# Kernel tuning notes

Hardware: AMD Instinct MI355X
Metric: run time of the kernel (lower is better)

Reference implementation:

```python
import jax, jax.numpy as jnp
import numpy as np

STATE_DIM = 256
LATENT_DIM = 64
HIDDEN = 64
NUM_EMB = 2048
BATCH = 32768


def setup_inputs() -> dict:
    key = jax.random.key(0)
    ks = jax.random.split(key, 10)
    s = lambda *sh: 1.0 / np.sqrt(sh[0])
    return {
        "x": jax.random.normal(ks[0], (BATCH, STATE_DIM), dtype=jnp.float32),
        # encoder: Linear(state_dim, 64) -> ReLU -> Linear(64, latent_dim)
        "enc_w1": jax.random.uniform(ks[1], (STATE_DIM, HIDDEN), jnp.float32, -s(STATE_DIM), s(STATE_DIM)),
        "enc_b1": jax.random.uniform(ks[2], (HIDDEN,), jnp.float32, -s(STATE_DIM), s(STATE_DIM)),
        "enc_w2": jax.random.uniform(ks[3], (HIDDEN, LATENT_DIM), jnp.float32, -s(HIDDEN), s(HIDDEN)),
        "enc_b2": jax.random.uniform(ks[4], (LATENT_DIM,), jnp.float32, -s(HIDDEN), s(HIDDEN)),
        # codebook
        "emb": jax.random.normal(ks[5], (NUM_EMB, LATENT_DIM), dtype=jnp.float32),
        # decoder: Linear(latent_dim, 64) -> ReLU -> Linear(64, state_dim)
        "dec_w1": jax.random.uniform(ks[6], (LATENT_DIM, HIDDEN), jnp.float32, -s(LATENT_DIM), s(LATENT_DIM)),
        "dec_b1": jax.random.uniform(ks[7], (HIDDEN,), jnp.float32, -s(LATENT_DIM), s(LATENT_DIM)),
        "dec_w2": jax.random.uniform(ks[8], (HIDDEN, STATE_DIM), jnp.float32, -s(HIDDEN), s(HIDDEN)),
        "dec_b2": jax.random.uniform(ks[9], (STATE_DIM,), jnp.float32, -s(HIDDEN), s(HIDDEN)),
    }


def reference(x, enc_w1, enc_b1, enc_w2, enc_b2, emb, dec_w1, dec_b1, dec_w2, dec_b2):
    # encoder MLP: z_e [B, latent]
    h = jax.nn.relu(x @ enc_w1 + enc_b1)
    z_e = h @ enc_w2 + enc_b2
    # squared euclidean distances to codebook, expanded form: [B, K]
    # ||z - e||^2 = ||z||^2 - 2 z.e + ||e||^2  (same argmin as broadcast form)
    d = (jnp.sum(z_e * z_e, axis=1, keepdims=True)
         - 2.0 * (z_e @ emb.T)
         + jnp.sum(emb * emb, axis=1)[None, :])
    z_q_idx = jnp.argmin(d, axis=1)           # [B]
    z_q = emb[z_q_idx]                        # [B, latent]
    # decoder MLP
    hd = jax.nn.relu(z_q @ dec_w1 + dec_b1)
    x_recon = hd @ dec_w2 + dec_b2
    return (x_recon, z_e, z_q)
```

## Files before the change

kernel.cpp:

```cpp
#include <hip/hip_runtime.h>

#define BATCH   32768
#define SD      256
#define LD      64
#define HDIM    64
#define NEMB    2048
#define REFINE_THR_Q 5e-4f

typedef short  short8 __attribute__((ext_vector_type(8)));
typedef float  f32x4  __attribute__((ext_vector_type(4)));

__device__ __forceinline__ unsigned short f2bf(float f) {
    unsigned int u = __float_as_uint(f);
    u = (u + 0x7FFFu + ((u >> 16) & 1u)) >> 16;
    return (unsigned short)u;
}
__device__ __forceinline__ float bf2f(unsigned short h) {
    return __uint_as_float(((unsigned int)h) << 16);
}

__global__ __launch_bounds__(256) void k0_all(const float* __restrict__ emb,
                                              const float* __restrict__ dw1,
                                              const float* __restrict__ dw2,
                                              float* __restrict__ e2q,
                                              unsigned short* __restrict__ eh,
                                              unsigned short* __restrict__ el,
                                              unsigned short* __restrict__ w1h,
                                              unsigned short* __restrict__ w1l,
                                              unsigned short* __restrict__ w2h,
                                              unsigned short* __restrict__ w2l,
                                              int* __restrict__ count) {
    int b = blockIdx.x;
    int t = threadIdx.x;
    if (b < 8) {
        int k = b * 256 + t;
        if (k == 0) *count = 0;
        const float* er = emb + (size_t)k * LD;
        unsigned short hrow[LD], lrow[LD];
        float s = 0.f;
#pragma unroll
        for (int q = 0; q < LD; ++q) {
            float v = er[q];
            s += v * v;
            unsigned short h = f2bf(v);
            hrow[q] = h;
            lrow[q] = f2bf(v - bf2f(h));
        }
        e2q[k] = -0.5f * s;
        short8* dh = (short8*)(eh + (size_t)k * LD);
        short8* dl = (short8*)(el + (size_t)k * LD);
#pragma unroll
        for (int q = 0; q < 8; ++q) {
            dh[q] = *(short8*)&hrow[q * 8];
            dl[q] = *(short8*)&lrow[q * 8];
        }
    } else if (b < 24) {
        int e = (b - 8) * 256 + t;
        int j = e >> 6, k = e & 63;
        float v = dw1[k * HDIM + j];
        unsigned short h = f2bf(v);
        w1h[e] = h; w1l[e] = f2bf(v - bf2f(h));
    } else {
        int e = (b - 24) * 256 + t;
        int j = e >> 6, k = e & 63;
        float v = dw2[k * SD + j];
        unsigned short h = f2bf(v);
        w2h[e] = h; w2l[e] = f2bf(v - bf2f(h));
    }
}

__global__ __launch_bounds__(512, 4) void k_enc(const float* __restrict__ x,
                                                const float* __restrict__ w1,
                                                const float* __restrict__ b1,
                                                const float* __restrict__ w2,
                                                const float* __restrict__ b2,
                                                float* __restrict__ zOut,
                                                unsigned short* __restrict__ zh,
                                                unsigned short* __restrict__ zl) {
    __shared__ float smem[20480];
    float* w1s = smem;
    float* xs  = smem + 16384;
    int tid = threadIdx.x;
    {
        const float4* src = (const float4*)w1;
        float4* dst = (float4*)w1s;
#pragma unroll
        for (int t = 0; t < 8; ++t) dst[tid + 512 * t] = src[tid + 512 * t];
    }
    int r0 = blockIdx.x * 64;
    int sr = tid >> 3;
    int sq = tid & 7;
    const float* xrow = x + (size_t)(r0 + sr) * SD + sq * 4;
    *(float4*)&xs[sr * 32 + sq * 4] = *(const float4*)xrow;
    __syncthreads();

    int lane = tid & 63;
    int w = tid >> 6;
    float acc[8];
#pragma unroll
    for (int r = 0; r < 8; ++r) acc[r] = 0.f;

    for (int c = 0; c < 8; ++c) {
        float4 nv;
        if (c < 7) nv = *(const float4*)(xrow + (c + 1) * 32);
        const float* xb = &xs[(c & 1) * 2048 + (w * 8) * 32];
        int kb = c * 32;
#pragma unroll
        for (int i0 = 0; i0 < 32; i0 += 8) {
            float wf[8];
#pragma unroll
            for (int jj = 0; jj < 8; ++jj) wf[jj] = w1s[(kb + i0 + jj) * HDIM + lane];
#pragma unroll
            for (int r = 0; r < 8; ++r) {
                const float* xr = xb + r * 32 + i0;
                float4 xa = *(const float4*)xr;
                float4 xc = *(const float4*)(xr + 4);
                acc[r] += xa.x * wf[0] + xa.y * wf[1] + xa.z * wf[2] + xa.w * wf[3]
                        + xc.x * wf[4] + xc.y * wf[5] + xc.z * wf[6] + xc.w * wf[7];
            }
        }
        __syncthreads();
        if (c < 7) *(float4*)&xs[((c + 1) & 1) * 2048 + sr * 32 + sq * 4] = nv;
        __syncthreads();
    }

    float* hs  = smem;
    float* w2s = smem + 4096;
    float bb1 = b1[lane];
#pragma unroll
    for (int r = 0; r < 8; ++r)
        hs[(w * 8 + r) * 64 + lane] = fmaxf(acc[r] + bb1, 0.f);
    {
        const float4* src = (const float4*)w2;
        float4* dst = (float4*)w2s;
        dst[tid] = src[tid];
        dst[tid + 512] = src[tid + 512];
    }
    __syncthreads();

    const float* hb = &hs[(w * 8) * 64];
    float ac2[8];
#pragma unroll
    for (int r = 0; r < 8; ++r) ac2[r] = 0.f;

    for (int j0 = 0; j0 < HDIM; j0 += 8) {
        float wf[8];
#pragma unroll
        for (int jj = 0; jj < 8; ++jj) wf[jj] = w2s[(j0 + jj) * LD + lane];
#pragma unroll
        for (int r = 0; r < 8; ++r) {
            const float* hr = hb + r * 64 + j0;
            float4 ha = *(const float4*)hr;
            float4 hc = *(const float4*)(hr + 4);
            ac2[r] += ha.x * wf[0] + ha.y * wf[1] + ha.z * wf[2] + ha.w * wf[3]
                    + hc.x * wf[4] + hc.y * wf[5] + hc.z * wf[6] + hc.w * wf[7];
        }
    }
    float bb2 = b2[lane];
#pragma unroll
    for (int r = 0; r < 8; ++r) {
        float z = ac2[r] + bb2;
        size_t o = (size_t)(r0 + w * 8 + r) * LD + lane;
        zOut[o] = z;
        unsigned short h = f2bf(z);
        zh[o] = h;
        zl[o] = f2bf(z - bf2f(h));
    }
}

#define K2_LOAD(P, t) do {                                                  \
    const unsigned short* ph_ = ehp + (size_t)(t) * 16 * LD;                \
    const unsigned short* pl_ = elp + (size_t)(t) * 16 * LD;                \
    P##a0 = *(const short8*)(ph_);                                          \
    P##a1 = *(const short8*)(ph_ + 32);                                     \
    P##a2 = *(const short8*)(pl_);                                          \
    P##a3 = *(const short8*)(pl_ + 32);                                     \
    P##e2 = *(const f32x4*)(e2q + cbase + (t) * 16 + hi * 4);               \
} while (0)

#define K2_COMP(P, t) do {                                                  \
    f32x4 acc_[4];                                                          \
    _Pragma("unroll")                                                       \
    for (int g = 0; g < 4; ++g) {                                           \
        f32x4 c_;                                                           \
        c_ = __builtin_amdgcn_mfma_f32_16x16x32_bf16(P##a0, bh[g][0], P##e2, 0, 0, 0); \
        c_ = __builtin_amdgcn_mfma_f32_16x16x32_bf16(P##a1, bh[g][1], c_, 0, 0, 0);    \
        c_ = __builtin_amdgcn_mfma_f32_16x16x32_bf16(P##a2, bh[g][0], c_, 0, 0, 0);    \
        c_ = __builtin_amdgcn_mfma_f32_16x16x32_bf16(P##a3, bh[g][1], c_, 0, 0, 0);    \
        c_ = __builtin_amdgcn_mfma_f32_16x16x32_bf16(P##a0, bl[g][0], c_, 0, 0, 0);    \
        c_ = __builtin_amdgcn_mfma_f32_16x16x32_bf16(P##a1, bl[g][1], c_, 0, 0, 0);    \
        acc_[g] = c_;                                                       \
    }                                                                       \
    _Pragma("unroll")                                                       \
    for (int g = 0; g < 4; ++g) {                                           \
        float m_ = fmaxf(fmaxf(acc_[g][0], acc_[g][1]),                     \
                         fmaxf(acc_[g][2], acc_[g][3]));                    \
        bool win_ = (m_ > bb[g]);                                           \
        qv[g] = win_ ? acc_[g] : qv[g];                                     \
        tt[g] = win_ ? (t) : tt[g];                                         \
        b2v[g] = fmaxf(b2v[g], fminf(bb[g], m_));                           \
        bb[g] = fmaxf(bb[g], m_);                                           \
    }                                                                       \
} while (0)

__global__ __launch_bounds__(256, 2) void k2_mfma(const unsigned short* __restrict__ zh,
                                                  const unsigned short* __restrict__ zl,
                                                  const unsigned short* __restrict__ eh,
                                                  const unsigned short* __restrict__ el,
                                                  const float* __restrict__ e2q,
                                                  int* __restrict__ idx,
                                                  int* __restrict__ list,
                                                  int* __restrict__ count) {
    int tid  = threadIdx.x;
    int lane = tid & 63;
    int w    = tid >> 6;
    int rb   = blockIdx.x * 64;
    int lo   = lane & 15;
    int hi   = lane >> 4;

    short8 bh[4][2], bl[4][2];
#pragma unroll
    for (int g = 0; g < 4; ++g) {
        size_t zo = (size_t)(rb + g * 16 + lo) * LD + hi * 8;
        bh[g][0] = *(const short8*)(zh + zo);
        bh[g][1] = *(const short8*)(zh + zo + 32);
        bl[g][0] = *(const short8*)(zl + zo);
        bl[g][1] = *(const short8*)(zl + zo + 32);
    }

    float bb[4], b2v[4];
    f32x4 qv[4];
    int   tt[4];
#pragma unroll
    for (int g = 0; g < 4; ++g) {
        bb[g] = -3.0e38f; b2v[g] = -3.0e38f; tt[g] = 0;
        qv[g][0] = qv[g][1] = qv[g][2] = qv[g][3] = -3.0e38f;
    }

    const int cbase = w * (NEMB / 4);
    const unsigned short* ehp = eh + (size_t)(cbase + lo) * LD + hi * 8;
    const unsigned short* elp = el + (size_t)(cbase + lo) * LD + hi * 8;

    short8 Aa0, Aa1, Aa2, Aa3; f32x4 Ae2;
    short8 Ba0, Ba1, Ba2, Ba3; f32x4 Be2;
    short8 Ca0, Ca1, Ca2, Ca3; f32x4 Ce2;

    K2_LOAD(A, 0);
    K2_LOAD(B, 1);
    K2_LOAD(C, 2);

    for (int tb = 0; tb < 27; tb += 3) {
        K2_COMP(A, tb);     K2_LOAD(A, tb + 3);
        K2_COMP(B, tb + 1); K2_LOAD(B, tb + 4);
        K2_COMP(C, tb + 2); K2_LOAD(C, tb + 5);
    }
    K2_COMP(A, 27); K2_LOAD(A, 30);
    K2_COMP(B, 28); K2_LOAD(B, 31);
    K2_COMP(C, 29);
    K2_COMP(A, 30);
    K2_COMP(B, 31);

    float ss[4];
    int   ii[4];
#pragma unroll
    for (int g = 0; g < 4; ++g) {
        float s0 = qv[g][0], s1 = qv[g][1], s2 = qv[g][2], s3 = qv[g][3];
        float M01 = fmaxf(s0, s1), L01 = fminf(s0, s1);
        float M23 = fmaxf(s2, s3), L23 = fminf(s2, s3);
        int   d01 = (s1 > s0) ? 1 : 0;
        int   d23 = (s3 > s2) ? 3 : 2;
        bool  cp  = (M23 > M01);
        float within2 = fmaxf(fminf(M01, M23), cp ? L23 : L01);
        int   dd  = cp ? d23 : d01;
        ii[g] = cbase + tt[g] * 16 + hi * 4 + dd;
        ss[g] = fmaxf(b2v[g], within2);
    }

#pragma unroll
    for (int off = 16; off <= 32; off <<= 1) {
#pragma unroll
        for (int g = 0; g < 4; ++g) {
            float ob = __shfl_xor(bb[g], off);
            float os = __shfl_xor(ss[g], off);
            int   oi = __shfl_xor(ii[g], off);
            ss[g] = fmaxf(fmaxf(fminf(bb[g], ob), os), ss[g]);
            ii[g] = (ob > bb[g]) ? oi : ii[g];
            bb[g] = fmaxf(bb[g], ob);
        }
    }

    __shared__ float Lb[4][64];
    __shared__ float Ls[4][64];
    __shared__ int   Li[4][64];
    if (lane < 16) {
#pragma unroll
        for (int g = 0; g < 4; ++g) {
            Lb[w][g * 16 + lane] = bb[g];
            Ls[w][g * 16 + lane] = ss[g];
            Li[w][g * 16 + lane] = ii[g];
        }
    }
    __syncthreads();

    if (tid < 64) {
        float B = Lb[0][tid], S = Ls[0][tid];
        int   I = Li[0][tid];
#pragma unroll
        for (int w2 = 1; w2 < 4; ++w2) {
            float ob = Lb[w2][tid], os = Ls[w2][tid];
            int   oi = Li[w2][tid];
            S = fmaxf(fmaxf(fminf(B, ob), os), S);
            I = (ob > B) ? oi : I;
            B = fmaxf(B, ob);
        }
        idx[rb + tid] = I;
        if (B - S < REFINE_THR_Q) {
            int p = atomicAdd(count, 1);
            list[p] = rb + tid;
        }
    }
}

__global__ __launch_bounds__(256) void k3_refine(const float* __restrict__ z,
                                                 const float* __restrict__ emb,
                                                 const int* __restrict__ count,
                                                 const int* __restrict__ list,
                                                 int* __restrict__ idx) {
    __shared__ double sv[256];
    __shared__ int    sx[256];
    int tid = threadIdx.x;
    int n = *count;
    for (int g = blockIdx.x; g < n; g += gridDim.x) {
        int row = list[g];
        const float4* zr4 = (const float4*)(z + (size_t)row * LD);
        float4 zv[16];
#pragma unroll
        for (int q = 0; q < 16; ++q) zv[q] = zr4[q];

        double best = 1.0e300;
        int bi = NEMB;
#pragma unroll 2
        for (int c = 0; c < 8; ++c) {
            int k = tid * 8 + c;
            const float4* er = (const float4*)(emb + (size_t)k * LD);
            double d0 = 0.0, d1 = 0.0, d2 = 0.0, d3 = 0.0;
#pragma unroll
            for (int q = 0; q < 16; ++q) {
                float4 e4 = er[q];
                double tx = (double)zv[q].x - (double)e4.x;
                double ty = (double)zv[q].y - (double)e4.y;
                double tz = (double)zv[q].z - (double)e4.z;
                double tw = (double)zv[q].w - (double)e4.w;
                d0 += tx * tx; d1 += ty * ty; d2 += tz * tz; d3 += tw * tw;
            }
            double d = (d0 + d1) + (d2 + d3);
            if (d < best) { best = d; bi = k; }
        }
        sv[tid] = best; sx[tid] = bi;
        __syncthreads();
        for (int s = 128; s > 0; s >>= 1) {
            if (tid < s) {
                if (sv[tid + s] < sv[tid] ||
                    (sv[tid + s] == sv[tid] && sx[tid + s] < sx[tid])) {
                    sv[tid] = sv[tid + s]; sx[tid] = sx[tid + s];
                }
            }
            __syncthreads();
        }
        if (tid == 0) idx[row] = sx[0];
        __syncthreads();
    }
}

__global__ __launch_bounds__(256, 2) void k_dec(const int* __restrict__ idx,
                                                const float* __restrict__ emb,
                                                const unsigned short* __restrict__ w1h,
                                                const unsigned short* __restrict__ w1l,
                                                const float* __restrict__ b1,
                                                const unsigned short* __restrict__ w2h,
                                                const unsigned short* __restrict__ w2l,
                                                const float* __restrict__ b2,
                                                float* __restrict__ xrec,
                                                float* __restrict__ zq) {
    __shared__ float hds[4][16 * 68];
    int tid  = threadIdx.x;
    int lane = tid & 63;
    int w    = tid >> 6;
    int lo   = lane & 15;
    int hi   = lane >> 4;
    int rb   = blockIdx.x * 64 + w * 16;
    int row  = rb + lo;
    int ix   = idx[row];

    short8 zah[2], zal[2];
    {
        const float* er  = emb + (size_t)ix * LD + hi * 8;
        float* zqr = zq + (size_t)row * LD + hi * 8;
#pragma unroll
        for (int kt = 0; kt < 2; ++kt) {
            float4 a = *(const float4*)(er + kt * 32);
            float4 b = *(const float4*)(er + kt * 32 + 4);
            *(float4*)(zqr + kt * 32) = a;
            *(float4*)(zqr + kt * 32 + 4) = b;
            float v[8] = {a.x, a.y, a.z, a.w, b.x, b.y, b.z, b.w};
            unsigned short hh[8], ll[8];
#pragma unroll
            for (int q = 0; q < 8; ++q) {
                unsigned short hb = f2bf(v[q]);
                hh[q] = hb;
                ll[q] = f2bf(v[q] - bf2f(hb));
            }
            zah[kt] = *(short8*)hh;
            zal[kt] = *(short8*)ll;
        }
    }

#pragma unroll
    for (int jt = 0; jt < 4; ++jt) {
        float bj = b1[jt * 16 + lo];
        f32x4 c = {bj, bj, bj, bj};
#pragma unroll
        for (int kt = 0; kt < 2; ++kt) {
            short8 bh8 = *(const short8*)(w1h + (jt * 16 + lo) * LD + kt * 32 + hi * 8);
            short8 bl8 = *(const short8*)(w1l + (jt * 16 + lo) * LD + kt * 32 + hi * 8);
            c = __builtin_amdgcn_mfma_f32_16x16x32_bf16(zah[kt], bh8, c, 0, 0, 0);
            c = __builtin_amdgcn_mfma_f32_16x16x32_bf16(zah[kt], bl8, c, 0, 0, 0);
            c = __builtin_amdgcn_mfma_f32_16x16x32_bf16(zal[kt], bh8, c, 0, 0, 0);
        }
#pragma unroll
        for (int r = 0; r < 4; ++r)
            hds[w][(hi * 4 + r) * 68 + jt * 16 + lo] = fmaxf(c[r], 0.f);
    }
    __syncthreads();

    short8 hah[2], hal[2];
#pragma unroll
    for (int kt = 0; kt < 2; ++kt) {
        float4 a = *(const float4*)&hds[w][lo * 68 + kt * 32 + hi * 8];
        float4 b = *(const float4*)&hds[w][lo * 68 + kt * 32 + hi * 8 + 4];
        float v[8] = {a.x, a.y, a.z, a.w, b.x, b.y, b.z, b.w};
        unsigned short hh[8], ll[8];
#pragma unroll
        for (int q = 0; q < 8; ++q) {
            unsigned short hb = f2bf(v[q]);
            hh[q] = hb;
            ll[q] = f2bf(v[q] - bf2f(hb));
        }
        hah[kt] = *(short8*)hh;
        hal[kt] = *(short8*)ll;
    }

    for (int jt = 0; jt < 16; ++jt) {
        float bj = b2[jt * 16 + lo];
        f32x4 c = {bj, bj, bj, bj};
#pragma unroll
        for (int kt = 0; kt < 2; ++kt) {
            short8 bh8 = *(const short8*)(w2h + (jt * 16 + lo) * LD + kt * 32 + hi * 8);
            short8 bl8 = *(const short8*)(w2l + (jt * 16 + lo) * LD + kt * 32 + hi * 8);
            c = __builtin_amdgcn_mfma_f32_16x16x32_bf16(hah[kt], bh8, c, 0, 0, 0);
            c = __builtin_amdgcn_mfma_f32_16x16x32_bf16(hah[kt], bl8, c, 0, 0, 0);
            c = __builtin_amdgcn_mfma_f32_16x16x32_bf16(hal[kt], bh8, c, 0, 0, 0);
        }
#pragma unroll
        for (int r = 0; r < 4; ++r)
            xrec[(size_t)(rb + hi * 4 + r) * SD + jt * 16 + lo] = c[r];
    }
}

extern "C" void kernel_launch(void* const* d_in, const int* in_sizes, int n_in,
                              void* d_out, int out_size, void* d_ws, size_t ws_size,
                              hipStream_t stream) {
    const float* x   = (const float*)d_in[0];
    const float* ew1 = (const float*)d_in[1];
    const float* eb1 = (const float*)d_in[2];
    const float* ew2 = (const float*)d_in[3];
    const float* eb2 = (const float*)d_in[4];
    const float* emb = (const float*)d_in[5];
    const float* dw1 = (const float*)d_in[6];
    const float* db1 = (const float*)d_in[7];
    const float* dw2 = (const float*)d_in[8];
    const float* db2 = (const float*)d_in[9];

    float* out  = (float*)d_out;
    float* xrec = out;
    float* zE   = out + (size_t)BATCH * SD;
    float* zQ   = zE + (size_t)BATCH * LD;

    char* xb = (char*)xrec;
    unsigned short* zh  = (unsigned short*)xb;
    unsigned short* zl  = (unsigned short*)(xb + (4u << 20));
    unsigned short* eh  = (unsigned short*)(xb + (8u << 20));
    unsigned short* el  = (unsigned short*)(xb + (8u << 20) + (NEMB * LD * 2));
    float*          e2q = (float*)(xb + (9u << 20));

    char* ws = (char*)d_ws;
    int*  count = (int*)ws;
    int*  idxA  = (int*)(ws + 16384);
    int*  list  = (int*)(ws + 147456);
    unsigned short* w1h = (unsigned short*)(ws + 278528);
    unsigned short* w1l = (unsigned short*)(ws + 286720);
    unsigned short* w2h = (unsigned short*)(ws + 294912);
    unsigned short* w2l = (unsigned short*)(ws + 327680);

    hipLaunchKernelGGL(k0_all,    dim3(88),         dim3(256), 0, stream,
                       emb, dw1, dw2, e2q, eh, el, w1h, w1l, w2h, w2l, count);
    hipLaunchKernelGGL(k_enc,     dim3(BATCH / 64), dim3(512), 0, stream, x, ew1, eb1, ew2, eb2, zE, zh, zl);
    hipLaunchKernelGGL(k2_mfma,   dim3(BATCH / 64), dim3(256), 0, stream, zh, zl, eh, el, e2q, idxA, list, count);
    hipLaunchKernelGGL(k3_refine, dim3(128),        dim3(256), 0, stream, zE, emb, count, list, idxA);
    hipLaunchKernelGGL(k_dec,     dim3(BATCH / 64), dim3(256), 0, stream, idxA, emb, w1h, w1l, db1, w2h, w2l, db2, xrec, zQ);
}
```

Before: 127.3 us.

## Move encoder MLP to bf16x3 MFMA and fold refinement into argmin kernel

Rewrites the encoder from scalar FP32 FMAs on LDS-staged weights to 16x16x32 bf16 MFMA. Inputs and weights are split into three bf16 parts and six cross products are summed, so the result stays close to FP32. Weight splitting is added to the prep kernel. The separate refine kernel and its global atomic list are removed; each argmin block now refines its own near-tie rows in place. This saves a launch and an atomic, but refinement work may be unevenly spread across blocks.

```diff
diff --git a/kernel.cpp b/kernel.cpp
--- a/kernel.cpp
+++ b/kernel.cpp
@@ -22,6 +22,8 @@
 __global__ __launch_bounds__(256) void k0_all(const float* __restrict__ emb,
                                               const float* __restrict__ dw1,
                                               const float* __restrict__ dw2,
+                                              const float* __restrict__ ew1,
+                                              const float* __restrict__ ew2,
                                               float* __restrict__ e2q,
                                               unsigned short* __restrict__ eh,
                                               unsigned short* __restrict__ el,
@@ -29,12 +31,16 @@
                                               unsigned short* __restrict__ w1l,
                                               unsigned short* __restrict__ w2h,
                                               unsigned short* __restrict__ w2l,
-                                              int* __restrict__ count) {
+                                              unsigned short* __restrict__ w1eh,
+                                              unsigned short* __restrict__ w1em,
+                                              unsigned short* __restrict__ w1el,
+                                              unsigned short* __restrict__ w2eh,
+                                              unsigned short* __restrict__ w2em,
+                                              unsigned short* __restrict__ w2el) {
     int b = blockIdx.x;
     int t = threadIdx.x;
     if (b < 8) {
         int k = b * 256 + t;
-        if (k == 0) *count = 0;
         const float* er = emb + (size_t)k * LD;
         unsigned short hrow[LD], lrow[LD];
         float s = 0.f;
@@ -60,111 +66,152 @@
         float v = dw1[k * HDIM + j];
         unsigned short h = f2bf(v);
         w1h[e] = h; w1l[e] = f2bf(v - bf2f(h));
-    } else {
+    } else if (b < 88) {
         int e = (b - 24) * 256 + t;
         int j = e >> 6, k = e & 63;
         float v = dw2[k * SD + j];
         unsigned short h = f2bf(v);
         w2h[e] = h; w2l[e] = f2bf(v - bf2f(h));
-    }
-}
-
-__global__ __launch_bounds__(512, 4) void k_enc(const float* __restrict__ x,
-                                                const float* __restrict__ w1,
+    } else if (b < 152) {
+        int e = (b - 88) * 256 + t;
+        int j = e >> 8, k = e & 255;
+        float v = ew1[k * HDIM + j];
+        unsigned short h = f2bf(v);
+        float r1 = v - bf2f(h);
+        unsigned short m = f2bf(r1);
+        float r2 = r1 - bf2f(m);
+        w1eh[e] = h; w1em[e] = m; w1el[e] = f2bf(r2);
+    } else {
+        int e = (b - 152) * 256 + t;
+        int j = e >> 6, k = e & 63;
+        float v = ew2[k * LD + j];
+        unsigned short h = f2bf(v);
+        float r1 = v - bf2f(h);
+        unsigned short m = f2bf(r1);
+        float r2 = r1 - bf2f(m);
+        w2eh[e] = h; w2em[e] = m; w2el[e] = f2bf(r2);
+    }
+}
+
+#define MF(Afr, Bfr, C) __builtin_amdgcn_mfma_f32_16x16x32_bf16(Afr, Bfr, C, 0, 0, 0)
+
+__global__ __launch_bounds__(256, 2) void k_enc(const float* __restrict__ x,
+                                                const unsigned short* __restrict__ w1eh,
+                                                const unsigned short* __restrict__ w1em,
+                                                const unsigned short* __restrict__ w1el,
                                                 const float* __restrict__ b1,
-                                                const float* __restrict__ w2,
+                                                const unsigned short* __restrict__ w2eh,
+                                                const unsigned short* __restrict__ w2em,
+                                                const unsigned short* __restrict__ w2el,
                                                 const float* __restrict__ b2,
                                                 float* __restrict__ zOut,
                                                 unsigned short* __restrict__ zh,
                                                 unsigned short* __restrict__ zl) {
-    __shared__ float smem[20480];
-    float* w1s = smem;
-    float* xs  = smem + 16384;
-    int tid = threadIdx.x;
-    {
-        const float4* src = (const float4*)w1;
-        float4* dst = (float4*)w1s;
-#pragma unroll
-        for (int t = 0; t < 8; ++t) dst[tid + 512 * t] = src[tid + 512 * t];
-    }
-    int r0 = blockIdx.x * 64;
-    int sr = tid >> 3;
-    int sq = tid & 7;
-    const float* xrow = x + (size_t)(r0 + sr) * SD + sq * 4;
-    *(float4*)&xs[sr * 32 + sq * 4] = *(const float4*)xrow;
+    __shared__ float hds[4][16 * 68];
+    int tid  = threadIdx.x;
+    int lane = tid & 63;
+    int w    = tid >> 6;
+    int lo   = lane & 15;
+    int hi   = lane >> 4;
+    int rb   = blockIdx.x * 64 + w * 16;
+    int row  = rb + lo;
+
+    f32x4 c1[4];
+#pragma unroll
+    for (int jt = 0; jt < 4; ++jt) {
+        float bj = b1[jt * 16 + lo];
+        f32x4 c = {bj, bj, bj, bj};
+        c1[jt] = c;
+    }
+
+#pragma unroll
+    for (int kt = 0; kt < 8; ++kt) {
+        const float* xp = x + (size_t)row * SD + kt * 32 + hi * 8;
+        float4 a4 = *(const float4*)xp;
+        float4 b4 = *(const float4*)(xp + 4);
+        float v[8] = {a4.x, a4.y, a4.z, a4.w, b4.x, b4.y, b4.z, b4.w};
+        unsigned short sh[8], sm[8], sl[8];
+#pragma unroll
+        for (int q = 0; q < 8; ++q) {
+            unsigned short h = f2bf(v[q]);
+            float r1 = v[q] - bf2f(h);
+            unsigned short m = f2bf(r1);
+            float r2 = r1 - bf2f(m);
+            sh[q] = h; sm[q] = m; sl[q] = f2bf(r2);
+        }
+        short8 ah = *(short8*)sh, am = *(short8*)sm, al = *(short8*)sl;
+#pragma unroll
+        for (int jt = 0; jt < 4; ++jt) {
+            size_t wo = (size_t)(jt * 16 + lo) * SD + kt * 32 + hi * 8;
+            short8 bh8 = *(const short8*)(w1eh + wo);
+            short8 bm8 = *(const short8*)(w1em + wo);
+            short8 bl8 = *(const short8*)(w1el + wo);
+            f32x4 c = c1[jt];
+            c = MF(al, bh8, c);
+            c = MF(am, bm8, c);
+            c = MF(ah, bl8, c);
+            c = MF(am, bh8, c);
+            c = MF(ah, bm8, c);
+            c = MF(ah, bh8, c);
+            c1[jt] = c;
+        }
+    }
+#pragma unroll
+    for (int jt = 0; jt < 4; ++jt)
+#pragma unroll
+        for (int r = 0; r < 4; ++r)
+            hds[w][(hi * 4 + r) * 68 + jt * 16 + lo] = fmaxf(c1[jt][r], 0.f);
     __syncthreads();
 
-    int lane = tid & 63;
-    int w = tid >> 6;
-    float acc[8];
-#pragma unroll
-    for (int r = 0; r < 8; ++r) acc[r] = 0.f;
-
-    for (int c = 0; c < 8; ++c) {
-        float4 nv;
-        if (c < 7) nv = *(const float4*)(xrow + (c + 1) * 32);
-        const float* xb = &xs[(c & 1) * 2048 + (w * 8) * 32];
-        int kb = c * 32;
-#pragma unroll
-        for (int i0 = 0; i0 < 32; i0 += 8) {
-            float wf[8];
-#pragma unroll
-            for (int jj = 0; jj < 8; ++jj) wf[jj] = w1s[(kb + i0 + jj) * HDIM + lane];
-#pragma unroll
-            for (int r = 0; r < 8; ++r) {
-                const float* xr = xb + r * 32 + i0;
-                float4 xa = *(const float4*)xr;
-                float4 xc = *(const float4*)(xr + 4);
-                acc[r] += xa.x * wf[0] + xa.y * wf[1] + xa.z * wf[2] + xa.w * wf[3]
-                        + xc.x * wf[4] + xc.y * wf[5] + xc.z * wf[6] + xc.w * wf[7];
-            }
-        }
-        __syncthreads();
-        if (c < 7) *(float4*)&xs[((c + 1) & 1) * 2048 + sr * 32 + sq * 4] = nv;
-        __syncthreads();
-    }
-
-    float* hs  = smem;
-    float* w2s = smem + 4096;
-    float bb1 = b1[lane];
-#pragma unroll
-    for (int r = 0; r < 8; ++r)
-        hs[(w * 8 + r) * 64 + lane] = fmaxf(acc[r] + bb1, 0.f);
-    {
-        const float4* src = (const float4*)w2;
-        float4* dst = (float4*)w2s;
-        dst[tid] = src[tid];
-        dst[tid + 512] = src[tid + 512];
-    }
-    __syncthreads();
-
-    const float* hb = &hs[(w * 8) * 64];
-    float ac2[8];
-#pragma unroll
-    for (int r = 0; r < 8; ++r) ac2[r] = 0.f;
-
-    for (int j0 = 0; j0 < HDIM; j0 += 8) {
-        float wf[8];
-#pragma unroll
-        for (int jj = 0; jj < 8; ++jj) wf[jj] = w2s[(j0 + jj) * LD + lane];
-#pragma unroll
-        for (int r = 0; r < 8; ++r) {
-            const float* hr = hb + r * 64 + j0;
-            float4 ha = *(const float4*)hr;
-            float4 hc = *(const float4*)(hr + 4);
-            ac2[r] += ha.x * wf[0] + ha.y * wf[1] + ha.z * wf[2] + ha.w * wf[3]
-                    + hc.x * wf[4] + hc.y * wf[5] + hc.z * wf[6] + hc.w * wf[7];
-        }
-    }
-    float bb2 = b2[lane];
-#pragma unroll
-    for (int r = 0; r < 8; ++r) {
-        float z = ac2[r] + bb2;
-        size_t o = (size_t)(r0 + w * 8 + r) * LD + lane;
-        zOut[o] = z;
-        unsigned short h = f2bf(z);
-        zh[o] = h;
-        zl[o] = f2bf(z - bf2f(h));
+    f32x4 c2[4];
+#pragma unroll
+    for (int jt = 0; jt < 4; ++jt) {
+        float bj = b2[jt * 16 + lo];
+        f32x4 c = {bj, bj, bj, bj};
+        c2[jt] = c;
+    }
+#pragma unroll
+    for (int kt = 0; kt < 2; ++kt) {
+        float4 a4 = *(const float4*)&hds[w][lo * 68 + kt * 32 + hi * 8];
+        float4 b4 = *(const float4*)&hds[w][lo * 68 + kt * 32 + hi * 8 + 4];
+        float v[8] = {a4.x, a4.y, a4.z, a4.w, b4.x, b4.y, b4.z, b4.w};
+        unsigned short sh[8], sm[8], sl[8];
+#pragma unroll
+        for (int q = 0; q < 8; ++q) {
+            unsigned short h = f2bf(v[q]);
+            float r1 = v[q] - bf2f(h);
+            unsigned short m = f2bf(r1);
+            float r2 = r1 - bf2f(m);
+            sh[q] = h; sm[q] = m; sl[q] = f2bf(r2);
+        }
+        short8 ah = *(short8*)sh, am = *(short8*)sm, al = *(short8*)sl;
+#pragma unroll
+        for (int jt = 0; jt < 4; ++jt) {
+            size_t wo = (size_t)(jt * 16 + lo) * LD + kt * 32 + hi * 8;
+            short8 bh8 = *(const short8*)(w2eh + wo);
+            short8 bm8 = *(const short8*)(w2em + wo);
+            short8 bl8 = *(const short8*)(w2el + wo);
+            f32x4 c = c2[jt];
+            c = MF(al, bh8, c);
+            c = MF(am, bm8, c);
+            c = MF(ah, bl8, c);
+            c = MF(am, bh8, c);
+            c = MF(ah, bm8, c);
+            c = MF(ah, bh8, c);
+            c2[jt] = c;
+        }
+    }
+#pragma unroll
+    for (int jt = 0; jt < 4; ++jt) {
+#pragma unroll
+        for (int r = 0; r < 4; ++r) {
+            float z = c2[jt][r];
+            size_t o = (size_t)(rb + hi * 4 + r) * LD + jt * 16 + lo;
+            zOut[o] = z;
+            unsigned short hb = f2bf(z);
+            zh[o] = hb;
+            zl[o] = f2bf(z - bf2f(hb));
+        }
     }
 }
 
@@ -208,9 +255,9 @@
                                                   const unsigned short* __restrict__ eh,
                                                   const unsigned short* __restrict__ el,
                                                   const float* __restrict__ e2q,
-                                                  int* __restrict__ idx,
-                                                  int* __restrict__ list,
-                                                  int* __restrict__ count) {
+                                                  const float* __restrict__ zE,
+                                                  const float* __restrict__ emb,
+                                                  int* __restrict__ idx) {
     int tid  = threadIdx.x;
     int lane = tid & 63;
     int w    = tid >> 6;
@@ -292,6 +339,7 @@
     __shared__ float Lb[4][64];
     __shared__ float Ls[4][64];
     __shared__ int   Li[4][64];
+    __shared__ int   flags[64];
     if (lane < 16) {
 #pragma unroll
         for (int g = 0; g < 4; ++g) {
@@ -314,29 +362,19 @@
             B = fmaxf(B, ob);
         }
         idx[rb + tid] = I;
-        if (B - S < REFINE_THR_Q) {
-            int p = atomicAdd(count, 1);
-            list[p] = rb + tid;
-        }
-    }
-}
-
-__global__ __launch_bounds__(256) void k3_refine(const float* __restrict__ z,
-                                                 const float* __restrict__ emb,
-                                                 const int* __restrict__ count,
-                                                 const int* __restrict__ list,
-                                                 int* __restrict__ idx) {
+        flags[tid] = (B - S < REFINE_THR_Q) ? 1 : 0;
+    }
+    __syncthreads();
+
     __shared__ double sv[256];
     __shared__ int    sx[256];
-    int tid = threadIdx.x;
-    int n = *count;
-    for (int g = blockIdx.x; g < n; g += gridDim.x) {
-        int row = list[g];
-        const float4* zr4 = (const float4*)(z + (size_t)row * LD);
+    for (int r = 0; r < 64; ++r) {
+        if (flags[r] == 0) continue;
+        int rrow = rb + r;
+        const float4* zr4 = (const float4*)(zE + (size_t)rrow * LD);
         float4 zv[16];
 #pragma unroll
         for (int q = 0; q < 16; ++q) zv[q] = zr4[q];
-
         double best = 1.0e300;
         int bi = NEMB;
 #pragma unroll 2
@@ -367,7 +405,7 @@
             }
             __syncthreads();
         }
-        if (tid == 0) idx[row] = sx[0];
+        if (tid == 0) idx[rrow] = sx[0];
         __syncthreads();
     }
 }
@@ -487,25 +525,32 @@
     float* zQ   = zE + (size_t)BATCH * LD;
 
     char* xb = (char*)xrec;
-    unsigned short* zh  = (unsigned short*)xb;
-    unsigned short* zl  = (unsigned short*)(xb + (4u << 20));
-    unsigned short* eh  = (unsigned short*)(xb + (8u << 20));
-    unsigned short* el  = (unsigned short*)(xb + (8u << 20) + (NEMB * LD * 2));
-    float*          e2q = (float*)(xb + (9u << 20));
+    unsigned short* zh   = (unsigned short*)xb;
+    unsigned short* zl   = (unsigned short*)(xb + (4u << 20));
+    unsigned short* eh   = (unsigned short*)(xb + (8u << 20));
+    unsigned short* el   = (unsigned short*)(xb + (8u << 20) + (NEMB * LD * 2));
+    float*          e2q  = (float*)(xb + (9u << 20));
+    unsigned short* w1eh = (unsigned short*)(xb + (10u << 20));
+    unsigned short* w1em = w1eh + 16384;
+    unsigned short* w1el = w1em + 16384;
+    unsigned short* w2eh = w1el + 16384;
+    unsigned short* w2em = w2eh + 4096;
+    unsigned short* w2el = w2em + 4096;
 
     char* ws = (char*)d_ws;
-    int*  count = (int*)ws;
     int*  idxA  = (int*)(ws + 16384);
-    int*  list  = (int*)(ws + 147456);
     unsigned short* w1h = (unsigned short*)(ws + 278528);
     unsigned short* w1l = (unsigned short*)(ws + 286720);
     unsigned short* w2h = (unsigned short*)(ws + 294912);
     unsigned short* w2l = (unsigned short*)(ws + 327680);
 
-    hipLaunchKernelGGL(k0_all,    dim3(88),         dim3(256), 0, stream,
-                       emb, dw1, dw2, e2q, eh, el, w1h, w1l, w2h, w2l, count);
-    hipLaunchKernelGGL(k_enc,     dim3(BATCH / 64), dim3(512), 0, stream, x, ew1, eb1, ew2, eb2, zE, zh, zl);
-    hipLaunchKernelGGL(k2_mfma,   dim3(BATCH / 64), dim3(256), 0, stream, zh, zl, eh, el, e2q, idxA, list, count);
-    hipLaunchKernelGGL(k3_refine, dim3(128),        dim3(256), 0, stream, zE, emb, count, list, idxA);
-    hipLaunchKernelGGL(k_dec,     dim3(BATCH / 64), dim3(256), 0, stream, idxA, emb, w1h, w1l, db1, w2h, w2l, db2, xrec, zQ);
-}
+    hipLaunchKernelGGL(k0_all,  dim3(168),        dim3(256), 0, stream,
+                       emb, dw1, dw2, ew1, ew2, e2q, eh, el,
+                       w1h, w1l, w2h, w2l, w1eh, w1em, w1el, w2eh, w2em, w2el);
+    hipLaunchKernelGGL(k_enc,   dim3(BATCH / 64), dim3(256), 0, stream,
+                       x, w1eh, w1em, w1el, eb1, w2eh, w2em, w2el, eb2, zE, zh, zl);
+    hipLaunchKernelGGL(k2_mfma, dim3(BATCH / 64), dim3(256), 0, stream,
+                       zh, zl, eh, el, e2q, zE, emb, idxA);
+    hipLaunchKernelGGL(k_dec,   dim3(BATCH / 64), dim3(256), 0, stream,
+                       idxA, emb, w1h, w1l, db1, w2h, w2l, db2, xrec, zQ);
+}
```

Result: no change. 128.7 us (+1.1%).
